# Performance work log

Hardware: AMD Instinct MI355X
Metric: run time of the kernel (lower is better)

Reference implementation:

```python
import jax, jax.numpy as jnp
import numpy as np

B, T, U, V = 8, 128, 100, 1024
BLANK = 0
NEG = -1e30  # safe -inf surrogate (finite grads through logaddexp)


def setup_inputs() -> dict:
    key = jax.random.key(0)
    k1, k2 = jax.random.split(key)
    logits = jax.random.normal(k1, (B, T, U + 1, V), dtype=jnp.float32)
    # targets drawn from non-blank ids [1, V)
    targets = jax.random.randint(k2, (B, U), 1, V, dtype=jnp.int32)
    logit_lengths = jnp.full((B,), T, dtype=jnp.int32)
    target_lengths = jnp.full((B,), U, dtype=jnp.int32)
    return {"logits": logits, "targets": targets,
            "logit_lengths": logit_lengths, "target_lengths": target_lengths}


def _rnnt_nll(log_probs, targets, t_len, u_len):
    """Negative log-likelihood of one utterance.
    log_probs: [T, U+1, V] (log-softmaxed joiner output), targets: [U] int.
    alpha[t,u] = logaddexp(alpha[t-1,u] + blank[t-1,u], alpha[t,u-1] + emit[t,u-1]).
    """
    blank_lp = log_probs[:, :, BLANK]                      # [T, U+1]
    emit_lp = log_probs[:, jnp.arange(U), targets]         # [T, U]

    # row t=0: pure emissions
    alpha0 = jnp.concatenate([jnp.zeros((1,), log_probs.dtype),
                              jnp.cumsum(emit_lp[0])])     # [U+1]

    def combine(x, y):
        # linear log-space recurrence x[u] = logaddexp(c[u], x[u-1] + a[u])
        a1, c1 = x
        a2, c2 = y
        return (a1 + a2, jnp.logaddexp(c2, c1 + a2))

    def step(prev_row, inp):
        blank_prev, emit_t = inp                           # [U+1], [U]
        c = prev_row + blank_prev                          # vertical (blank) moves
        a = jnp.concatenate([jnp.full((1,), NEG, log_probs.dtype), emit_t])
        _, row = jax.lax.associative_scan(combine, (a, c))
        return row, row

    _, rows = jax.lax.scan(step, alpha0, (blank_lp[:-1], emit_lp[1:]))
    alpha = jnp.concatenate([alpha0[None, :], rows], axis=0)  # [T, U+1]

    ll = alpha[t_len - 1, u_len] + blank_lp[t_len - 1, u_len]
    return -ll


def reference(logits, targets, logit_lengths, target_lengths):
    log_probs = jax.nn.log_softmax(logits, axis=-1)
    # module passes src_lengths - 1 to rnnt_loss
    t_lens = logit_lengths - 1
    nll = jax.vmap(_rnnt_nll)(log_probs, targets, t_lens, target_lengths)
    return jnp.mean(nll)  # reduction='mean'
```

## Files before the change

kernel.cpp:

```cpp
#include <hip/hip_runtime.h>


constexpr int Bb = 8;
constexpr int Tt = 128;
constexpr int Uu = 100;
constexpr int Vv = 1024;
constexpr int UP1 = Uu + 1;
constexpr int DROWS = 244;
constexpr int DPAD  = 104;
constexpr int LROWS = 233;
constexpr int REG   = 29;
constexpr int NREG  = 8;

__device__ __forceinline__ unsigned short f2bf(float f) {
    unsigned int u = __builtin_bit_cast(unsigned int, f);
    u += 0x7fffu + ((u >> 16) & 1u);
    return (unsigned short)(u >> 16);
}
__device__ __forceinline__ float bflo(unsigned int p) {
    return __builtin_bit_cast(float, p << 16);
}
__device__ __forceinline__ float bfhi(unsigned int p) {
    return __builtin_bit_cast(float, p & 0xffff0000u);
}

__device__ __forceinline__ float wave_shr1(float x) {
    return __builtin_bit_cast(float, __builtin_amdgcn_update_dpp(
        0, __builtin_bit_cast(int, x), 0x138, 0xf, 0xf, true));
}

__device__ __forceinline__ float readlane_f(float x, int lane) {
    return __builtin_bit_cast(float,
        __builtin_amdgcn_readlane(__builtin_bit_cast(int, x), lane));
}

#define DPP_MAXSTEP(x, ctrl, rmask) {                                        \
    float _t = __builtin_bit_cast(float, __builtin_amdgcn_update_dpp(        \
        __builtin_bit_cast(int, x), __builtin_bit_cast(int, x),              \
        ctrl, rmask, 0xf, false));                                           \
    x = fmaxf(x, _t); }
#define WAVE_SCAN_MAX(x)           \
    DPP_MAXSTEP(x, 0x111, 0xf);    \
    DPP_MAXSTEP(x, 0x112, 0xf);    \
    DPP_MAXSTEP(x, 0x114, 0xf);    \
    DPP_MAXSTEP(x, 0x118, 0xf);    \
    DPP_MAXSTEP(x, 0x142, 0xa);    \
    DPP_MAXSTEP(x, 0x143, 0xc)

__global__ __launch_bounds__(256) void lse_kernel(
        const float* __restrict__ logits,
        const int*   __restrict__ targets,
        unsigned short* __restrict__ bS,
        unsigned short* __restrict__ eS) {
    const int wid  = blockIdx.x * 4 + (threadIdx.x >> 6);
    const int lane = threadIdx.x & 63;
    const int b   = wid / (Tt * UP1);
    const int rem = wid - b * (Tt * UP1);
    const int t   = rem / UP1;
    const int u   = rem - t * UP1;

    const float* row = logits + (size_t)wid * Vv;
    const float4* r4 = (const float4*)row;
    float4 x0 = r4[lane];
    float4 x1 = r4[lane + 64];
    float4 x2 = r4[lane + 128];
    float4 x3 = r4[lane + 192];

    float m = fmaxf(fmaxf(fmaxf(x0.x, x0.y), fmaxf(x0.z, x0.w)),
                    fmaxf(fmaxf(x1.x, x1.y), fmaxf(x1.z, x1.w)));
    m = fmaxf(m, fmaxf(fmaxf(fmaxf(x2.x, x2.y), fmaxf(x2.z, x2.w)),
                       fmaxf(fmaxf(x3.x, x3.y), fmaxf(x3.z, x3.w))));
    #pragma unroll
    for (int d = 32; d > 0; d >>= 1) m = fmaxf(m, __shfl_xor(m, d, 64));

    float s = __expf(x0.x - m) + __expf(x0.y - m) + __expf(x0.z - m) + __expf(x0.w - m)
            + __expf(x1.x - m) + __expf(x1.y - m) + __expf(x1.z - m) + __expf(x1.w - m)
            + __expf(x2.x - m) + __expf(x2.y - m) + __expf(x2.z - m) + __expf(x2.w - m)
            + __expf(x3.x - m) + __expf(x3.y - m) + __expf(x3.z - m) + __expf(x3.w - m);
    #pragma unroll
    for (int d = 32; d > 0; d >>= 1) s += __shfl_xor(s, d, 64);

    float lse = m + __logf(s);

    if (lane == 0) {
        const int dw = t + u + 1;
        bS[((size_t)b * DROWS + dw) * DPAD + u] = f2bf(__expf(x0.x - lse));
        if (u < Uu) {
            int tgt = targets[b * Uu + u];
            eS[((size_t)b * DROWS + dw) * DPAD + (u + 1)] = f2bf(__expf(row[tgt] - lse));
        }
    }
}

__global__ __launch_bounds__(576) void dp_kernel(
        const unsigned short* __restrict__ bS,
        const unsigned short* __restrict__ eS,
        const int* __restrict__ logit_lengths,
        const int* __restrict__ target_lengths,
        float* __restrict__ nll) {
    const int b    = blockIdx.x;
    const int tid  = threadIdx.x;
    const int wvi  = tid >> 6;
    const int lane = tid & 63;

    __shared__ __align__(16) unsigned short lB[LROWS][DPAD];
    __shared__ __align__(16) unsigned short lE[LROWS][DPAD];
    __shared__ int sflag[NREG];

    if (tid < NREG) sflag[tid] = 0;
    __syncthreads();

    const size_t bstride = (size_t)DROWS * DPAD;

    if (wvi >= 1) {
        const int w = wvi - 1;
        const int row0 = 1 + REG * w;
        constexpr int RBYTES = REG * DPAD * 2;
        const char* gb = (const char*)(bS + (size_t)b * bstride + (size_t)row0 * DPAD);
        const char* ge = (const char*)(eS + (size_t)b * bstride + (size_t)row0 * DPAD);
        char* db = (char*)&lB[row0][0];
        char* de = (char*)&lE[row0][0];
        for (int k = lane * 16; k < RBYTES; k += 64 * 16) {
            *(uint4*)(db + k) = *(const uint4*)(gb + k);
            *(uint4*)(de + k) = *(const uint4*)(ge + k);
        }
        if (lane < REG) {
            const int d = row0 + lane;
            lB[d][101] = 0; lB[d][102] = 0; lB[d][103] = 0;
            lE[d][0] = 0; lE[d][101] = 0; lE[d][102] = 0; lE[d][103] = 0;
        }
        __hip_atomic_store(&sflag[w], 1, __ATOMIC_RELEASE,
                           __HIP_MEMORY_SCOPE_WORKGROUP);
        return;
    }

    const int tl = logit_lengths[b];
    const int ul = target_lengths[b];
    const int t_idx = tl - 2;
    const int dcap  = t_idx + ul;

    const int u0 = lane * 2;

    float P0 = (lane == 0) ? 1.0f : 0.0f;
    float P1 = 0.0f;
    float S  = 0.0f;
    float capP = (dcap == 0) ? 1.0f : 0.0f;
    float capS = 0.0f;

#define STEP(dv, ub, ue) do {                                          \
        float Bx = bflo(ub), By = bfhi(ub);                            \
        float Ex = bflo(ue), Ey = bfhi(ue);                            \
        float sh = wave_shr1(P1);                                      \
        float n1 = fmaf(P1, By, P0 * Ey);                              \
        float n0 = fmaf(P0, Bx, sh * Ex);                              \
        P0 = n0; P1 = n1;                                              \
        if ((dv) == dcap) {                                            \
            float w0 = readlane_f(n0, ul >> 1);                        \
            float w1 = readlane_f(n1, ul >> 1);                        \
            capP = (ul & 1) ? w1 : w0;                                 \
            capS = S;                                                  \
        }                                                              \
    } while (0)

#define RESCALE do {                                                   \
        float gm = fmaxf(P0, P1);                                      \
        WAVE_SCAN_MAX(gm);                                             \
        float mm = readlane_f(gm, 63);                                 \
        float rr = 1.0f / mm;                                          \
        P0 *= rr; P1 *= rr;                                            \
        S += __logf(mm);                                               \
    } while (0)

#define GROUP(N, JOFF) do {                                            \
        unsigned int ub[N], ue[N];                                     \
        _Pragma("unroll")                                              \
        for (int r = 0; r < (N); ++r) {                                \
            ub[r] = *(const unsigned int*)&lB[dbase + (JOFF) + r][u0]; \
            ue[r] = *(const unsigned int*)&lE[dbase + (JOFF) + r][u0]; \
        }                                                              \
        _Pragma("unroll")                                              \
        for (int r = 0; r < (N); ++r)                                  \
            STEP(dbase + (JOFF) + r, ub[r], ue[r]);                    \
        RESCALE;                                                       \
    } while (0)

    for (int w = 0; w < NREG; ++w) {
        while (__hip_atomic_load(&sflag[w], __ATOMIC_ACQUIRE,
                                 __HIP_MEMORY_SCOPE_WORKGROUP) == 0)
            __builtin_amdgcn_s_sleep(1);
        __builtin_amdgcn_sched_barrier(0);

        const int dbase = 1 + REG * w;
        GROUP(8, 0); GROUP(8, 8); GROUP(8, 16); GROUP(5, 24);
    }
#undef GROUP
#undef RESCALE
#undef STEP

    if (lane == 0) {
        unsigned short hv = lB[dcap + 1][ul];
        float blk = __builtin_bit_cast(float, ((unsigned int)hv) << 16);
        nll[b] = -(__logf(capP) + capS + __logf(blk));
    }
}

__global__ void mean_kernel(const float* __restrict__ nll, float* __restrict__ out) {
    if (threadIdx.x == 0 && blockIdx.x == 0) {
        float s = 0.0f;
        for (int i = 0; i < Bb; ++i) s += nll[i];
        out[0] = s / (float)Bb;
    }
}

extern "C" void kernel_launch(void* const* d_in, const int* in_sizes, int n_in,
                              void* d_out, int out_size, void* d_ws, size_t ws_size,
                              hipStream_t stream) {
    const float* logits         = (const float*)d_in[0];
    const int*   targets        = (const int*)d_in[1];
    const int*   logit_lengths  = (const int*)d_in[2];
    const int*   target_lengths = (const int*)d_in[3];
    float* out = (float*)d_out;

    unsigned short* bS = (unsigned short*)d_ws;
    unsigned short* eS = bS + (size_t)Bb * DROWS * DPAD;
    float* nll = (float*)(eS + (size_t)Bb * DROWS * DPAD);

    const int rows = Bb * Tt * UP1;
    lse_kernel<<<rows / 4, 256, 0, stream>>>(logits, targets, bS, eS);
    dp_kernel<<<Bb, 576, 0, stream>>>(bS, eS, logit_lengths, target_lengths, nll);
    mean_kernel<<<1, 64, 0, stream>>>(nll, out);
}
```

Measured before the change: 92.73 us.

## Run DP recurrence in packed bf16, software-pipeline LDS loads, fold mean into DP kernel

The anti-diagonal DP state is now held as packed bf16x2 and updated with hfma2/hmul2, with the neighbour shift done by DPP plus alignbit instead of separate fp32 lanes. LDS row loads are double-buffered across groups of eight diagonals, and readiness flags are checked per group rather than per region. The separate mean kernel is removed: the last DP block to finish, tracked by an atomic counter, computes the mean. The bf16 arithmetic in the recurrence loses precision and could let errors build up over the 228 diagonals. The counter is reset from inside lse_kernel.

```diff
diff --git a/kernel.cpp b/kernel.cpp
--- a/kernel.cpp
+++ b/kernel.cpp
@@ -1,4 +1,5 @@
 #include <hip/hip_runtime.h>
+#include <hip/hip_bf16.h>
 
 
 constexpr int Bb = 8;
@@ -23,15 +24,28 @@
 __device__ __forceinline__ float bfhi(unsigned int p) {
     return __builtin_bit_cast(float, p & 0xffff0000u);
 }
-
-__device__ __forceinline__ float wave_shr1(float x) {
-    return __builtin_bit_cast(float, __builtin_amdgcn_update_dpp(
-        0, __builtin_bit_cast(int, x), 0x138, 0xf, 0xf, true));
+__device__ __forceinline__ __hip_bfloat162 u2bf(unsigned int p) {
+    __hip_bfloat162 h;
+    __builtin_memcpy(&h, &p, sizeof(h));
+    return h;
+}
+__device__ __forceinline__ unsigned int bf2u(__hip_bfloat162 h) {
+    unsigned int p;
+    __builtin_memcpy(&p, &h, sizeof(p));
+    return p;
+}
+
+__device__ __forceinline__ unsigned int shr1u(unsigned int x) {
+    return (unsigned int)__builtin_amdgcn_update_dpp(
+        0, (int)x, 0x138, 0xf, 0xf, true);
 }
 
 __device__ __forceinline__ float readlane_f(float x, int lane) {
     return __builtin_bit_cast(float,
         __builtin_amdgcn_readlane(__builtin_bit_cast(int, x), lane));
+}
+__device__ __forceinline__ unsigned int readlane_u(unsigned int x, int lane) {
+    return (unsigned int)__builtin_amdgcn_readlane((int)x, lane);
 }
 
 #define DPP_MAXSTEP(x, ctrl, rmask) {                                        \
@@ -51,7 +65,11 @@
         const float* __restrict__ logits,
         const int*   __restrict__ targets,
         unsigned short* __restrict__ bS,
-        unsigned short* __restrict__ eS) {
+        unsigned short* __restrict__ eS,
+        int* __restrict__ dcnt) {
+    if (blockIdx.x == 0 && threadIdx.x == 0)
+        __hip_atomic_store(dcnt, 0, __ATOMIC_RELAXED, __HIP_MEMORY_SCOPE_AGENT);
+
     const int wid  = blockIdx.x * 4 + (threadIdx.x >> 6);
     const int lane = threadIdx.x & 63;
     const int b   = wid / (Tt * UP1);
@@ -97,7 +115,9 @@
         const unsigned short* __restrict__ eS,
         const int* __restrict__ logit_lengths,
         const int* __restrict__ target_lengths,
-        float* __restrict__ nll) {
+        float* __restrict__ nll,
+        int*   __restrict__ dcnt,
+        float* __restrict__ out) {
     const int b    = blockIdx.x;
     const int tid  = threadIdx.x;
     const int wvi  = tid >> 6;
@@ -141,74 +161,94 @@
 
     const int u0 = lane * 2;
 
-    float P0 = (lane == 0) ? 1.0f : 0.0f;
-    float P1 = 0.0f;
+    unsigned int Pu = (lane == 0) ? 0x00003F80u : 0u;
     float S  = 0.0f;
-    float capP = (dcap == 0) ? 1.0f : 0.0f;
+    unsigned int capPu = (dcap == 0) ? 0x00003F80u : 0u;
     float capS = 0.0f;
 
-#define STEP(dv, ub, ue) do {                                          \
-        float Bx = bflo(ub), By = bfhi(ub);                            \
-        float Ex = bflo(ue), Ey = bfhi(ue);                            \
-        float sh = wave_shr1(P1);                                      \
-        float n1 = fmaf(P1, By, P0 * Ey);                              \
-        float n0 = fmaf(P0, Bx, sh * Ex);                              \
-        P0 = n0; P1 = n1;                                              \
-        if ((dv) == dcap) {                                            \
-            float w0 = readlane_f(n0, ul >> 1);                        \
-            float w1 = readlane_f(n1, ul >> 1);                        \
-            capP = (ul & 1) ? w1 : w0;                                 \
-            capS = S;                                                  \
+#define PSTEP(dv, ubv, uev) do {                                       \
+        unsigned int shP = shr1u(Pu);                                  \
+        unsigned int M = __builtin_amdgcn_alignbit(Pu, shP, 16);       \
+        Pu = bf2u(__hfma2(u2bf(ubv), u2bf(Pu),                         \
+                          __hmul2(u2bf(uev), u2bf(M))));               \
+        if ((dv) == dcap) { capPu = Pu; capS = S; }                    \
+    } while (0)
+
+#define RESCALE do {                                                   \
+        float p0 = bflo(Pu), p1 = bfhi(Pu);                            \
+        float gm = fmaxf(p0, p1);                                      \
+        WAVE_SCAN_MAX(gm);                                             \
+        float mm = fmaxf(readlane_f(gm, 63), 1e-30f);                  \
+        float rr = 1.0f / mm;                                          \
+        unsigned short rh = f2bf(rr);                                  \
+        unsigned int rp = ((unsigned int)rh << 16) | rh;               \
+        Pu = bf2u(__hmul2(u2bf(Pu), u2bf(rp)));                        \
+        S += __logf(mm);                                               \
+    } while (0)
+
+#define LOADG(UB, UE, k) do {                                          \
+        _Pragma("unroll")                                              \
+        for (int r = 0; r < 8; ++r) {                                  \
+            UB[r] = *(const unsigned int*)&lB[(k) * 8 + 1 + r][u0];    \
+            UE[r] = *(const unsigned int*)&lE[(k) * 8 + 1 + r][u0];    \
         }                                                              \
     } while (0)
 
-#define RESCALE do {                                                   \
-        float gm = fmaxf(P0, P1);                                      \
-        WAVE_SCAN_MAX(gm);                                             \
-        float mm = readlane_f(gm, 63);                                 \
-        float rr = 1.0f / mm;                                          \
-        P0 *= rr; P1 *= rr;                                            \
-        S += __logf(mm);                                               \
-    } while (0)
-
-#define GROUP(N, JOFF) do {                                            \
-        unsigned int ub[N], ue[N];                                     \
+#define COMPG(UB, UE, k) do {                                          \
         _Pragma("unroll")                                              \
-        for (int r = 0; r < (N); ++r) {                                \
-            ub[r] = *(const unsigned int*)&lB[dbase + (JOFF) + r][u0]; \
-            ue[r] = *(const unsigned int*)&lE[dbase + (JOFF) + r][u0]; \
+        for (int r = 0; r < 8; ++r)                                    \
+            PSTEP((k) * 8 + 1 + r, UB[r], UE[r]);                      \
+        RESCALE;                                                       \
+    } while (0)
+
+    int wcur = -1;
+#define ENSURE(wn) do {                                                \
+        while (wcur < (wn)) {                                          \
+            ++wcur;                                                    \
+            while (__hip_atomic_load(&sflag[wcur], __ATOMIC_ACQUIRE,   \
+                       __HIP_MEMORY_SCOPE_WORKGROUP) == 0)             \
+                __builtin_amdgcn_s_sleep(1);                           \
         }                                                              \
-        _Pragma("unroll")                                              \
-        for (int r = 0; r < (N); ++r)                                  \
-            STEP(dbase + (JOFF) + r, ub[r], ue[r]);                    \
-        RESCALE;                                                       \
-    } while (0)
-
-    for (int w = 0; w < NREG; ++w) {
-        while (__hip_atomic_load(&sflag[w], __ATOMIC_ACQUIRE,
-                                 __HIP_MEMORY_SCOPE_WORKGROUP) == 0)
-            __builtin_amdgcn_s_sleep(1);
-        __builtin_amdgcn_sched_barrier(0);
-
-        const int dbase = 1 + REG * w;
-        GROUP(8, 0); GROUP(8, 8); GROUP(8, 16); GROUP(5, 24);
-    }
-#undef GROUP
+    } while (0)
+
+    unsigned int Ab[8], Ae[8], Bb_[8], Be_[8];
+    ENSURE(7 / REG);
+    LOADG(Ab, Ae, 0);
+    for (int c = 0; c < 14; ++c) {
+        const int k0 = 2 * c, k1 = 2 * c + 1;
+        ENSURE((8 * k1 + 7) / REG);
+        LOADG(Bb_, Be_, k1);
+        COMPG(Ab, Ae, k0);
+        if (k1 < 28) {
+            ENSURE((8 * (k1 + 1) + 7) / REG);
+            LOADG(Ab, Ae, k1 + 1);
+        }
+        COMPG(Bb_, Be_, k1);
+    }
+    COMPG(Ab, Ae, 28);
+#undef PSTEP
 #undef RESCALE
-#undef STEP
+#undef LOADG
+#undef COMPG
+#undef ENSURE
+
+    unsigned int cw = readlane_u(capPu, ul >> 1);
+    float capv = (ul & 1) ? bfhi(cw) : bflo(cw);
 
     if (lane == 0) {
-        unsigned short hv = lB[dcap + 1][ul];
-        float blk = __builtin_bit_cast(float, ((unsigned int)hv) << 16);
-        nll[b] = -(__logf(capP) + capS + __logf(blk));
-    }
-}
-
-__global__ void mean_kernel(const float* __restrict__ nll, float* __restrict__ out) {
-    if (threadIdx.x == 0 && blockIdx.x == 0) {
-        float s = 0.0f;
-        for (int i = 0; i < Bb; ++i) s += nll[i];
-        out[0] = s / (float)Bb;
+        float blk = __builtin_bit_cast(float, ((unsigned int)lB[dcap + 1][ul]) << 16);
+        float ll = __logf(capv) + capS + __logf(blk);
+        __hip_atomic_store(&nll[b], -ll, __ATOMIC_RELEASE,
+                           __HIP_MEMORY_SCOPE_AGENT);
+        int prev = __hip_atomic_fetch_add(dcnt, 1, __ATOMIC_ACQ_REL,
+                                          __HIP_MEMORY_SCOPE_AGENT);
+        if (prev == Bb - 1) {
+            float s = 0.0f;
+            for (int i = 0; i < Bb; ++i)
+                s += __hip_atomic_load(&nll[i], __ATOMIC_ACQUIRE,
+                                       __HIP_MEMORY_SCOPE_AGENT);
+            out[0] = s / (float)Bb;
+        }
     }
 }
 
@@ -221,12 +261,13 @@
     const int*   target_lengths = (const int*)d_in[3];
     float* out = (float*)d_out;
 
-    unsigned short* bS = (unsigned short*)d_ws;
+    int* dcnt = (int*)d_ws;
+    unsigned short* bS = (unsigned short*)d_ws + 8;
     unsigned short* eS = bS + (size_t)Bb * DROWS * DPAD;
     float* nll = (float*)(eS + (size_t)Bb * DROWS * DPAD);
 
     const int rows = Bb * Tt * UP1;
-    lse_kernel<<<rows / 4, 256, 0, stream>>>(logits, targets, bS, eS);
-    dp_kernel<<<Bb, 576, 0, stream>>>(bS, eS, logit_lengths, target_lengths, nll);
-    mean_kernel<<<1, 64, 0, stream>>>(nll, out);
-}
+    lse_kernel<<<rows / 4, 256, 0, stream>>>(logits, targets, bS, eS, dcnt);
+    dp_kernel<<<Bb, 576, 0, stream>>>(bS, eS, logit_lengths, target_lengths,
+                                      nll, dcnt, out);
+}
```

Result: slower. 97.06 us (+4.7%).
